# Kernel optimization log

Measured on AMD Instinct MI355X. Metric: run time of the kernel, lower is better.

The kernel has to match this reference:

```python
import jax, jax.numpy as jnp
import numpy as np

B, S, D, H = 4, 2048, 1024, 16
DK = D // H
EPS = 1e-5


def setup_inputs() -> dict:
    key = jax.random.key(0)
    ks = jax.random.split(key, 9)
    lim = 1.0 / np.sqrt(DK)  # nn.Linear default init range
    def u(k, shape):
        return jax.random.uniform(k, shape, jnp.float32, -lim, lim)
    return {
        "x": jax.random.normal(ks[0], (B, S, D), jnp.float32),
        "Wq": u(ks[1], (H, DK, DK)),
        "bq": u(ks[2], (H, DK)),
        "Wk": u(ks[3], (H, DK, DK)),
        "bk": u(ks[4], (H, DK)),
        "Wv": u(ks[5], (H, DK, DK)),
        "bv": u(ks[6], (H, DK)),
        "gamma": jnp.ones((D,), jnp.float32),
        "beta": jnp.zeros((D,), jnp.float32),
    }


def reference(x, Wq, bq, Wk, bk, Wv, bv, gamma, beta):
    b, s, d = x.shape
    h, dk = Wq.shape[0], Wq.shape[1]
    xh = x.reshape(b, s, h, dk)  # chunk along feature dim -> per-head slices
    # per-head linear projections (heads batched into one einsum)
    Q = jnp.einsum("bshd,hde->bshe", xh, Wq) + bq
    K = jnp.einsum("bshd,hde->bshe", xh, Wk) + bk
    V = jnp.einsum("bshd,hde->bshe", xh, Wv) + bv
    scale = jnp.sqrt(jnp.asarray(dk, x.dtype))
    scores = jnp.einsum("bshe,bthe->bhst", Q, K) / scale  # [B,H,S,S]
    causal = jnp.tril(jnp.ones((s, s), bool))  # apply_mask=True
    scores = jnp.where(causal, scores, -jnp.inf)
    P = jax.nn.softmax(scores, axis=-1)
    O = jnp.einsum("bhst,bthe->bshe", P, V).reshape(b, s, d)  # concat heads
    # dropout is identity in eval mode; residual + LayerNorm
    y = O + x
    mu = jnp.mean(y, axis=-1, keepdims=True)
    var = jnp.mean(jnp.square(y - mu), axis=-1, keepdims=True)
    return (y - mu) * jax.lax.rsqrt(var + EPS) * gamma + beta
```

## Files before the change

kernel.cpp:

```cpp
#include <hip/hip_runtime.h>
#include <hip/hip_bf16.h>

typedef __bf16 bf16_t;
typedef bf16_t bf16x8 __attribute__((ext_vector_type(8)));
typedef bf16_t bf16x4 __attribute__((ext_vector_type(4)));
typedef float f32x4 __attribute__((ext_vector_type(4)));

#define SEQ    2048
#define DHEAD  64
#define DMODEL 1024
#define KVB    64
#define BHN    64
#define LOG2E  1.4426950408889634f

__device__ __forceinline__ f32x4 mfma16(bf16x8 a, bf16x8 b, f32x4 c) {
  return __builtin_amdgcn_mfma_f32_16x16x32_bf16(a, b, c, 0, 0, 0);
}

__device__ __forceinline__ void gload16(void* l, const void* g) {
  __builtin_amdgcn_global_load_lds(
      (const __attribute__((address_space(1))) unsigned int*)g,
      (__attribute__((address_space(3))) unsigned int*)l,
      16, 0, 0);
}

__global__ __launch_bounds__(256) void qkv_kernel(
    const float* __restrict__ x,
    const float* __restrict__ Wq, const float* __restrict__ bq,
    const float* __restrict__ Wk, const float* __restrict__ bk,
    const float* __restrict__ Wv, const float* __restrict__ bv,
    bf16_t* __restrict__ Qw, bf16_t* __restrict__ Kw, bf16_t* __restrict__ VTw) {
  __shared__ __align__(16) char x_lds[256 * 128];
  __shared__ __align__(16) char w_lds[8192];

  const int bh = blockIdx.y;
  const int b = bh >> 4, h = bh & 15;
  const int s0 = blockIdx.x * 256;
  const int t = threadIdx.x;
  const int w = t >> 6, lane = t & 63;
  const int lo = lane & 15, g = lane >> 4;

#pragma unroll
  for (int p = 0; p < 8; ++p) {
    const int row = p * 32 + (t >> 3);
    const int c = t & 7;
    const float* xp = x + ((size_t)(b * SEQ + s0 + row)) * DMODEL + h * DHEAD + c * 8;
    const float4 f0 = *(const float4*)xp;
    const float4 f1 = *(const float4*)(xp + 4);
    bf16x8 v;
    v[0] = (bf16_t)f0.x; v[1] = (bf16_t)f0.y; v[2] = (bf16_t)f0.z; v[3] = (bf16_t)f0.w;
    v[4] = (bf16_t)f1.x; v[5] = (bf16_t)f1.y; v[6] = (bf16_t)f1.z; v[7] = (bf16_t)f1.w;
    *(bf16x8*)(x_lds + row * 128 + ((c * 16) ^ ((row & 7) << 4))) = v;
  }
  __syncthreads();

  for (int wi = 0; wi < 3; ++wi) {
    const float* Wp = (wi == 0) ? Wq : (wi == 1) ? Wk : Wv;
    const float* Bp = (wi == 0) ? bq : (wi == 1) ? bk : bv;
    bf16_t* Op      = (wi == 0) ? Qw : Kw;

    if (wi > 0) __syncthreads();
    {
      const int d = t >> 2, e0 = (t & 3) * 16;
      const float* wp = Wp + (size_t)(h * 64 + d) * 64 + e0;
      const float4 f0 = *(const float4*)(wp);
      const float4 f1 = *(const float4*)(wp + 4);
      const float4 f2 = *(const float4*)(wp + 8);
      const float4 f3 = *(const float4*)(wp + 12);
      float vals[16];
      vals[0] = f0.x; vals[1] = f0.y; vals[2] = f0.z; vals[3] = f0.w;
      vals[4] = f1.x; vals[5] = f1.y; vals[6] = f1.z; vals[7] = f1.w;
      vals[8] = f2.x; vals[9] = f2.y; vals[10] = f2.z; vals[11] = f2.w;
      vals[12] = f3.x; vals[13] = f3.y; vals[14] = f3.z; vals[15] = f3.w;
#pragma unroll
      for (int j = 0; j < 16; ++j) {
        const int e = e0 + j;
        *(bf16_t*)(w_lds + e * 128 + ((2 * d) ^ ((e & 7) << 4))) = (bf16_t)vals[j];
      }
    }
    __syncthreads();

    bf16x8 wf[2][4];
#pragma unroll
    for (int ct = 0; ct < 4; ++ct)
#pragma unroll
      for (int ks = 0; ks < 2; ++ks)
        wf[ks][ct] = *(const bf16x8*)(w_lds + (ct * 16 + lo) * 128 +
                                      ((ks * 64 + g * 16) ^ ((lo & 7) << 4)));
    float4 biasv[4];
    float biass[4];
    if (wi < 2) {
#pragma unroll
      for (int ct = 0; ct < 4; ++ct)
        biasv[ct] = *(const float4*)(Bp + h * 64 + ct * 16 + g * 4);
    } else {
#pragma unroll
      for (int ct = 0; ct < 4; ++ct) biass[ct] = Bp[h * 64 + ct * 16 + lo];
    }

    const float sc = (wi == 0) ? (0.125f * LOG2E) : 1.0f;
#pragma unroll
    for (int it = 0; it < 4; ++it) {
      const int r0 = it * 64 + w * 16;
      bf16x8 xa[2];
#pragma unroll
      for (int ks = 0; ks < 2; ++ks) {
        const int row = r0 + lo;
        xa[ks] = *(const bf16x8*)(x_lds + row * 128 +
                                  ((ks * 64 + g * 16) ^ ((row & 7) << 4)));
      }
      if (wi < 2) {
#pragma unroll
        for (int ct = 0; ct < 4; ++ct) {
          f32x4 a = (f32x4){0.f, 0.f, 0.f, 0.f};
          a = mfma16(wf[0][ct], xa[0], a);
          a = mfma16(wf[1][ct], xa[1], a);
          bf16x4 pk;
#pragma unroll
          for (int r = 0; r < 4; ++r)
            pk[r] = (bf16_t)((a[r] + ((const float*)&biasv[ct])[r]) * sc);
          *(bf16x4*)(Op + ((size_t)bh * SEQ + s0 + r0 + lo) * DHEAD + ct * 16 + g * 4) = pk;
        }
      } else {
#pragma unroll
        for (int ct = 0; ct < 4; ++ct) {
          f32x4 a = (f32x4){0.f, 0.f, 0.f, 0.f};
          a = mfma16(xa[0], wf[0][ct], a);
          a = mfma16(xa[1], wf[1][ct], a);
          bf16x4 pk;
#pragma unroll
          for (int r = 0; r < 4; ++r) pk[r] = (bf16_t)(a[r] + biass[ct]);
          *(bf16x4*)(VTw + ((size_t)bh * DHEAD + ct * 16 + lo) * SEQ + s0 + r0 + g * 4) = pk;
        }
      }
    }
  }
}

__global__ __launch_bounds__(256, 4) void attn_kernel(
    const bf16_t* __restrict__ Qw, const bf16_t* __restrict__ Kw,
    const bf16_t* __restrict__ VTw, float* __restrict__ Out) {
  __shared__ __align__(16) char stage_lds[2][16384];
  __shared__ __align__(16) char p_lds[4][2048];

  const int f = blockIdx.x;
  const int bh = (f & 7) * 8 + ((f >> 3) & 7);
  const int pair = f >> 6;
  const int b = bh >> 4, h = bh & 15;

  const int t = threadIdx.x;
  const int w = t >> 6, lane = t & 63;
  const int lo = lane & 15, g = lane >> 4;
  char* pbase = &p_lds[w][0];

  const int strow = w * 8 + (lane >> 3);
  const int scol = ((lane & 7) * 16) ^ ((lane >> 3) << 4);
  const char* Kbase = (const char*)(Kw + (size_t)bh * SEQ * DHEAD);
  const char* Vbase = (const char*)(VTw + (size_t)bh * DHEAD * SEQ);
  const bf16_t* Qb = Qw + (size_t)bh * SEQ * DHEAD;
  const int swz = (lo & 7) << 4;

  for (int half = 0; half < 2; ++half) {
    const int qt = half ? (31 - pair) : pair;
    const int q0 = qt * 64;
    const int qw0 = q0 + w * 16;
    const int kts = qt + 1;

    bf16x8 qf[2];
    {
      const bf16_t* qp = Qb + (size_t)(qw0 + lo) * DHEAD + g * 8;
      qf[0] = *(const bf16x8*)(qp);
      qf[1] = *(const bf16x8*)(qp + 32);
    }
    float m_run = -1e30f, l_run = 0.f;
    f32x4 oacc[4];
#pragma unroll
    for (int dt = 0; dt < 4; ++dt) oacc[dt] = (f32x4){0.f, 0.f, 0.f, 0.f};

    __syncthreads();
    {
      char* db = &stage_lds[0][0];
#pragma unroll
      for (int p = 0; p < 2; ++p) {
        gload16(db + p * 4096 + w * 1024,
                Kbase + (size_t)(p * 32 + strow) * 128 + scol);
        gload16(db + 8192 + p * 4096 + w * 1024,
                Vbase + (size_t)(p * 32 + strow) * 4096 + scol);
      }
    }
    int cur = 0;
    for (int kt = 0; kt < kts; ++kt) {
      const int kv0 = kt * KVB;
      __syncthreads();
      if (kt + 1 < kts) {
        const int nk = kv0 + KVB;
        char* db = &stage_lds[cur ^ 1][0];
#pragma unroll
        for (int p = 0; p < 2; ++p) {
          gload16(db + p * 4096 + w * 1024,
                  Kbase + (size_t)(nk + p * 32 + strow) * 128 + scol);
          gload16(db + 8192 + p * 4096 + w * 1024,
                  Vbase + (size_t)(p * 32 + strow) * 4096 + (size_t)nk * 2 + scol);
        }
      }
      const char* kb = &stage_lds[cur][0];
      const char* vb = kb + 8192;

      bf16x8 kf[2][4];
#pragma unroll
      for (int ks = 0; ks < 2; ++ks)
#pragma unroll
        for (int ct = 0; ct < 4; ++ct)
          kf[ks][ct] = *(const bf16x8*)(kb + (ct * 16 + lo) * 128 +
                                        ((ks * 64 + g * 16) ^ swz));
      f32x4 sa[4];
      __builtin_amdgcn_s_setprio(1);
#pragma unroll
      for (int ct = 0; ct < 4; ++ct) {
        f32x4 a = (f32x4){0.f, 0.f, 0.f, 0.f};
        a = mfma16(kf[0][ct], qf[0], a);
        a = mfma16(kf[1][ct], qf[1], a);
        sa[ct] = a;
      }
      __builtin_amdgcn_s_setprio(0);

      if (kt == qt) {
        const int q = qw0 + lo;
#pragma unroll
        for (int ct = 0; ct < 4; ++ct)
#pragma unroll
          for (int r = 0; r < 4; ++r) {
            const int kv = kv0 + ct * 16 + g * 4 + r;
            if (kv > q) sa[ct][r] = -1e30f;
          }
      }
      float mt = -1e30f;
#pragma unroll
      for (int ct = 0; ct < 4; ++ct)
        mt = fmaxf(mt, fmaxf(fmaxf(sa[ct][0], sa[ct][1]),
                             fmaxf(sa[ct][2], sa[ct][3])));
      mt = fmaxf(mt, __shfl_xor(mt, 16));
      mt = fmaxf(mt, __shfl_xor(mt, 32));
      if (__any(mt > m_run + 8.f)) {
        const float mn = fmaxf(m_run, mt);
        const float rs = exp2f(m_run - mn);
        l_run *= rs;
        m_run = mn;
#pragma unroll
        for (int r = 0; r < 4; ++r) {
          const float fr = __shfl(rs, g * 4 + r);
#pragma unroll
          for (int dt = 0; dt < 4; ++dt) oacc[dt][r] *= fr;
        }
      }
      float lt = 0.f;
#pragma unroll
      for (int ct = 0; ct < 4; ++ct) {
        bf16x4 pk;
#pragma unroll
        for (int r = 0; r < 4; ++r) {
          const float pv = exp2f(sa[ct][r] - m_run);
          lt += pv;
          pk[r] = (bf16_t)pv;
        }
        *(bf16x4*)(pbase + lo * 128 + ((ct * 32 + g * 8) ^ swz)) = pk;
      }
      lt += __shfl_xor(lt, 16);
      lt += __shfl_xor(lt, 32);
      l_run += lt;

      bf16x8 vf[2][4];
#pragma unroll
      for (int ks = 0; ks < 2; ++ks)
#pragma unroll
        for (int dt = 0; dt < 4; ++dt)
          vf[ks][dt] = *(const bf16x8*)(vb + (dt * 16 + lo) * 128 +
                                        ((ks * 64 + g * 16) ^ swz));
      __builtin_amdgcn_s_setprio(1);
#pragma unroll
      for (int ks = 0; ks < 2; ++ks) {
        const bf16x8 pa = *(const bf16x8*)(pbase + lo * 128 + ((ks * 64 + g * 16) ^ swz));
#pragma unroll
        for (int dt = 0; dt < 4; ++dt)
          oacc[dt] = mfma16(pa, vf[ks][dt], oacc[dt]);
      }
      __builtin_amdgcn_s_setprio(0);
      cur ^= 1;
    }
    const float inv = 1.f / l_run;
#pragma unroll
    for (int r = 0; r < 4; ++r) {
      const float fr = __shfl(inv, g * 4 + r);
      const int srow = qw0 + g * 4 + r;
      float* op = Out + ((size_t)b * SEQ + srow) * DMODEL + h * DHEAD;
#pragma unroll
      for (int dt = 0; dt < 4; ++dt) op[dt * 16 + lo] = oacc[dt][r] * fr;
    }
  }
}

__global__ __launch_bounds__(256) void ln_kernel(
    const float* __restrict__ x, const float* __restrict__ gamma,
    const float* __restrict__ beta, float* __restrict__ out) {
  __shared__ float red[8];
  const int row = blockIdx.x;
  const int t = threadIdx.x;
  float* orow = out + (size_t)row * DMODEL;
  const float* xrow = x + (size_t)row * DMODEL;

  const float4 o = *(const float4*)(orow + t * 4);
  const float4 xv = *(const float4*)(xrow + t * 4);
  float y0 = o.x + xv.x, y1 = o.y + xv.y, y2 = o.z + xv.z, y3 = o.w + xv.w;
  float s = y0 + y1 + y2 + y3;
  float sq = y0 * y0 + y1 * y1 + y2 * y2 + y3 * y3;
#pragma unroll
  for (int m = 1; m < 64; m <<= 1) {
    s += __shfl_xor(s, m);
    sq += __shfl_xor(sq, m);
  }
  const int w = t >> 6;
  if ((t & 63) == 0) { red[w] = s; red[4 + w] = sq; }
  __syncthreads();
  const float S = red[0] + red[1] + red[2] + red[3];
  const float SQ = red[4] + red[5] + red[6] + red[7];
  const float mu = S * (1.f / DMODEL);
  const float var = SQ * (1.f / DMODEL) - mu * mu;
  const float rstd = rsqrtf(var + 1e-5f);
  const float4 gv = *(const float4*)(gamma + t * 4);
  const float4 bv = *(const float4*)(beta + t * 4);
  float4 res;
  res.x = (y0 - mu) * rstd * gv.x + bv.x;
  res.y = (y1 - mu) * rstd * gv.y + bv.y;
  res.z = (y2 - mu) * rstd * gv.z + bv.z;
  res.w = (y3 - mu) * rstd * gv.w + bv.w;
  *(float4*)(orow + t * 4) = res;
}

extern "C" void kernel_launch(void* const* d_in, const int* in_sizes, int n_in,
                              void* d_out, int out_size, void* d_ws, size_t ws_size,
                              hipStream_t stream) {
  const float* x     = (const float*)d_in[0];
  const float* Wq    = (const float*)d_in[1];
  const float* bq    = (const float*)d_in[2];
  const float* Wk    = (const float*)d_in[3];
  const float* bk    = (const float*)d_in[4];
  const float* Wv    = (const float*)d_in[5];
  const float* bv    = (const float*)d_in[6];
  const float* gamma = (const float*)d_in[7];
  const float* beta  = (const float*)d_in[8];
  float* out = (float*)d_out;

  const size_t per = (size_t)BHN * SEQ * DHEAD;
  bf16_t* Qw  = (bf16_t*)d_ws;
  bf16_t* Kw  = Qw + per;
  bf16_t* VTw = Kw + per;

  qkv_kernel<<<dim3(8, 64), 256, 0, stream>>>(x, Wq, bq, Wk, bk, Wv, bv, Qw, Kw, VTw);
  attn_kernel<<<dim3(1024), 256, 0, stream>>>(Qw, Kw, VTw, out);
  ln_kernel<<<dim3(8192), 256, 0, stream>>>(x, gamma, beta, out);
}
```

Baseline: 198.9 us.

## Switch attention to 32x32 MFMA with 128-row query tiles and register-resident P

The attention kernel moves from 16x16x32 to 32x32x16 bf16 MFMA, with each wave owning 32 query rows. Query tiles grow to 128 rows, so the grid halves and launch bounds drop to 2 blocks per CU. P stays in registers via cvt_pk_bf16 and permlane32_swap instead of a round trip through LDS, and fully masked 32-column sub-blocks are skipped. The QKV kernel also preloads all three weight matrices into LDS up front to remove the per-weight barriers, at the cost of more LDS and registers, which lowers occupancy.

```diff
diff --git a/kernel.cpp b/kernel.cpp
--- a/kernel.cpp
+++ b/kernel.cpp
@@ -5,16 +5,29 @@
 typedef bf16_t bf16x8 __attribute__((ext_vector_type(8)));
 typedef bf16_t bf16x4 __attribute__((ext_vector_type(4)));
 typedef float f32x4 __attribute__((ext_vector_type(4)));
+typedef float f32x16 __attribute__((ext_vector_type(16)));
+typedef unsigned int u32;
+typedef u32 u32x4 __attribute__((ext_vector_type(4)));
 
 #define SEQ    2048
 #define DHEAD  64
 #define DMODEL 1024
-#define KVB    64
 #define BHN    64
 #define LOG2E  1.4426950408889634f
+#define NEGBIG (-1e30f)
+#define MASKV  (-1e38f)
 
 __device__ __forceinline__ f32x4 mfma16(bf16x8 a, bf16x8 b, f32x4 c) {
   return __builtin_amdgcn_mfma_f32_16x16x32_bf16(a, b, c, 0, 0, 0);
+}
+__device__ __forceinline__ f32x16 mfma32(bf16x8 a, bf16x8 b, f32x16 c) {
+  return __builtin_amdgcn_mfma_f32_32x32x16_bf16(a, b, c, 0, 0, 0);
+}
+__device__ __forceinline__ f32x16 zero16() {
+  f32x16 z;
+#pragma unroll
+  for (int i = 0; i < 16; ++i) z[i] = 0.f;
+  return z;
 }
 
 __device__ __forceinline__ void gload16(void* l, const void* g) {
@@ -31,7 +44,7 @@
     const float* __restrict__ Wv, const float* __restrict__ bv,
     bf16_t* __restrict__ Qw, bf16_t* __restrict__ Kw, bf16_t* __restrict__ VTw) {
   __shared__ __align__(16) char x_lds[256 * 128];
-  __shared__ __align__(16) char w_lds[8192];
+  __shared__ __align__(16) char w_lds[3][8192];
 
   const int bh = blockIdx.y;
   const int b = bh >> 4, h = bh & 15;
@@ -40,6 +53,26 @@
   const int w = t >> 6, lane = t & 63;
   const int lo = lane & 15, g = lane >> 4;
 
+#pragma unroll
+  for (int wi = 0; wi < 3; ++wi) {
+    const float* Wp = (wi == 0) ? Wq : (wi == 1) ? Wk : Wv;
+    const int d = t >> 2, e0 = (t & 3) * 16;
+    const float* wp = Wp + (size_t)(h * 64 + d) * 64 + e0;
+    const float4 f0 = *(const float4*)(wp);
+    const float4 f1 = *(const float4*)(wp + 4);
+    const float4 f2 = *(const float4*)(wp + 8);
+    const float4 f3 = *(const float4*)(wp + 12);
+    float vals[16];
+    vals[0] = f0.x; vals[1] = f0.y; vals[2] = f0.z; vals[3] = f0.w;
+    vals[4] = f1.x; vals[5] = f1.y; vals[6] = f1.z; vals[7] = f1.w;
+    vals[8] = f2.x; vals[9] = f2.y; vals[10] = f2.z; vals[11] = f2.w;
+    vals[12] = f3.x; vals[13] = f3.y; vals[14] = f3.z; vals[15] = f3.w;
+#pragma unroll
+    for (int j = 0; j < 16; ++j) {
+      const int e = e0 + j;
+      *(bf16_t*)(w_lds[wi] + e * 128 + ((2 * d) ^ ((e & 7) << 4))) = (bf16_t)vals[j];
+    }
+  }
 #pragma unroll
   for (int p = 0; p < 8; ++p) {
     const int row = p * 32 + (t >> 3);
@@ -54,38 +87,17 @@
   }
   __syncthreads();
 
+#pragma unroll
   for (int wi = 0; wi < 3; ++wi) {
-    const float* Wp = (wi == 0) ? Wq : (wi == 1) ? Wk : Wv;
     const float* Bp = (wi == 0) ? bq : (wi == 1) ? bk : bv;
     bf16_t* Op      = (wi == 0) ? Qw : Kw;
 
-    if (wi > 0) __syncthreads();
-    {
-      const int d = t >> 2, e0 = (t & 3) * 16;
-      const float* wp = Wp + (size_t)(h * 64 + d) * 64 + e0;
-      const float4 f0 = *(const float4*)(wp);
-      const float4 f1 = *(const float4*)(wp + 4);
-      const float4 f2 = *(const float4*)(wp + 8);
-      const float4 f3 = *(const float4*)(wp + 12);
-      float vals[16];
-      vals[0] = f0.x; vals[1] = f0.y; vals[2] = f0.z; vals[3] = f0.w;
-      vals[4] = f1.x; vals[5] = f1.y; vals[6] = f1.z; vals[7] = f1.w;
-      vals[8] = f2.x; vals[9] = f2.y; vals[10] = f2.z; vals[11] = f2.w;
-      vals[12] = f3.x; vals[13] = f3.y; vals[14] = f3.z; vals[15] = f3.w;
-#pragma unroll
-      for (int j = 0; j < 16; ++j) {
-        const int e = e0 + j;
-        *(bf16_t*)(w_lds + e * 128 + ((2 * d) ^ ((e & 7) << 4))) = (bf16_t)vals[j];
-      }
-    }
-    __syncthreads();
-
     bf16x8 wf[2][4];
 #pragma unroll
     for (int ct = 0; ct < 4; ++ct)
 #pragma unroll
       for (int ks = 0; ks < 2; ++ks)
-        wf[ks][ct] = *(const bf16x8*)(w_lds + (ct * 16 + lo) * 128 +
+        wf[ks][ct] = *(const bf16x8*)(w_lds[wi] + (ct * 16 + lo) * 128 +
                                       ((ks * 64 + g * 16) ^ ((lo & 7) << 4)));
     float4 biasv[4];
     float biass[4];
@@ -137,11 +149,10 @@
   }
 }
 
-__global__ __launch_bounds__(256, 4) void attn_kernel(
+__global__ __launch_bounds__(256, 2) void attn_kernel(
     const bf16_t* __restrict__ Qw, const bf16_t* __restrict__ Kw,
     const bf16_t* __restrict__ VTw, float* __restrict__ Out) {
   __shared__ __align__(16) char stage_lds[2][16384];
-  __shared__ __align__(16) char p_lds[4][2048];
 
   const int f = blockIdx.x;
   const int bh = (f & 7) * 8 + ((f >> 3) & 7);
@@ -150,152 +161,177 @@
 
   const int t = threadIdx.x;
   const int w = t >> 6, lane = t & 63;
-  const int lo = lane & 15, g = lane >> 4;
-  char* pbase = &p_lds[w][0];
-
-  const int strow = w * 8 + (lane >> 3);
-  const int scol = ((lane & 7) * 16) ^ ((lane >> 3) << 4);
+  const int l31 = lane & 31, hi = lane >> 5;
+
   const char* Kbase = (const char*)(Kw + (size_t)bh * SEQ * DHEAD);
   const char* Vbase = (const char*)(VTw + (size_t)bh * DHEAD * SEQ);
   const bf16_t* Qb = Qw + (size_t)bh * SEQ * DHEAD;
-  const int swz = (lo & 7) << 4;
 
   for (int half = 0; half < 2; ++half) {
-    const int qt = half ? (31 - pair) : pair;
-    const int q0 = qt * 64;
-    const int qw0 = q0 + w * 16;
-    const int kts = qt + 1;
-
-    bf16x8 qf[2];
-    {
-      const bf16_t* qp = Qb + (size_t)(qw0 + lo) * DHEAD + g * 8;
-      qf[0] = *(const bf16x8*)(qp);
-      qf[1] = *(const bf16x8*)(qp + 32);
-    }
-    float m_run = -1e30f, l_run = 0.f;
-    f32x4 oacc[4];
-#pragma unroll
-    for (int dt = 0; dt < 4; ++dt) oacc[dt] = (f32x4){0.f, 0.f, 0.f, 0.f};
+    const int qt = half ? (15 - pair) : pair;
+    const int qw0 = qt * 128 + w * 32;
+    const int qabs = qw0 + l31;
+    const int kts = 2 * qt + 2;
+
+    bf16x8 qf[4];
+#pragma unroll
+    for (int kk = 0; kk < 4; ++kk)
+      qf[kk] = *(const bf16x8*)(Qb + (size_t)qabs * DHEAD + kk * 16 + hi * 8);
+
+    float m = NEGBIG, l = 0.f;
+    f32x16 oacc[2];
+    oacc[0] = zero16();
+    oacc[1] = zero16();
 
     __syncthreads();
     {
       char* db = &stage_lds[0][0];
 #pragma unroll
       for (int p = 0; p < 2; ++p) {
-        gload16(db + p * 4096 + w * 1024,
-                Kbase + (size_t)(p * 32 + strow) * 128 + scol);
-        gload16(db + 8192 + p * 4096 + w * 1024,
-                Vbase + (size_t)(p * 32 + strow) * 4096 + scol);
+        const int c = w * 2 + p;
+        gload16(db + c * 1024, Kbase + (size_t)lane * 128 + c * 16);
+        gload16(db + 8192 + c * 1024, Vbase + (size_t)lane * 4096 + c * 16);
       }
     }
     int cur = 0;
     for (int kt = 0; kt < kts; ++kt) {
-      const int kv0 = kt * KVB;
+      const int kv0 = kt * 64;
       __syncthreads();
       if (kt + 1 < kts) {
-        const int nk = kv0 + KVB;
         char* db = &stage_lds[cur ^ 1][0];
+        const int nk = kv0 + 64;
 #pragma unroll
         for (int p = 0; p < 2; ++p) {
-          gload16(db + p * 4096 + w * 1024,
-                  Kbase + (size_t)(nk + p * 32 + strow) * 128 + scol);
-          gload16(db + 8192 + p * 4096 + w * 1024,
-                  Vbase + (size_t)(p * 32 + strow) * 4096 + (size_t)nk * 2 + scol);
-        }
-      }
+          const int c = w * 2 + p;
+          gload16(db + c * 1024, Kbase + (size_t)(nk + lane) * 128 + c * 16);
+          gload16(db + 8192 + c * 1024,
+                  Vbase + (size_t)lane * 4096 + (size_t)nk * 2 + c * 16);
+        }
+      }
+      const bool live0 = (kv0 <= qw0 + 31);
+      const bool live1 = (kv0 + 32 <= qw0 + 31);
+      if (!live0) { cur ^= 1; continue; }
       const char* kb = &stage_lds[cur][0];
       const char* vb = kb + 8192;
 
-      bf16x8 kf[2][4];
-#pragma unroll
-      for (int ks = 0; ks < 2; ++ks)
-#pragma unroll
-        for (int ct = 0; ct < 4; ++ct)
-          kf[ks][ct] = *(const bf16x8*)(kb + (ct * 16 + lo) * 128 +
-                                        ((ks * 64 + g * 16) ^ swz));
-      f32x4 sa[4];
+      f32x16 sa0 = zero16(), sa1 = zero16();
       __builtin_amdgcn_s_setprio(1);
 #pragma unroll
-      for (int ct = 0; ct < 4; ++ct) {
-        f32x4 a = (f32x4){0.f, 0.f, 0.f, 0.f};
-        a = mfma16(kf[0][ct], qf[0], a);
-        a = mfma16(kf[1][ct], qf[1], a);
-        sa[ct] = a;
+      for (int kk = 0; kk < 4; ++kk) {
+        const bf16x8 kf = *(const bf16x8*)(kb + (kk * 2 + hi) * 1024 + l31 * 16);
+        sa0 = mfma32(kf, qf[kk], sa0);
+      }
+      if (live1) {
+#pragma unroll
+        for (int kk = 0; kk < 4; ++kk) {
+          const bf16x8 kf = *(const bf16x8*)(kb + (kk * 2 + hi) * 1024 + (32 + l31) * 16);
+          sa1 = mfma32(kf, qf[kk], sa1);
+        }
       }
       __builtin_amdgcn_s_setprio(0);
 
-      if (kt == qt) {
-        const int q = qw0 + lo;
-#pragma unroll
-        for (int ct = 0; ct < 4; ++ct)
-#pragma unroll
-          for (int r = 0; r < 4; ++r) {
-            const int kv = kv0 + ct * 16 + g * 4 + r;
-            if (kv > q) sa[ct][r] = -1e30f;
-          }
-      }
-      float mt = -1e30f;
-#pragma unroll
-      for (int ct = 0; ct < 4; ++ct)
-        mt = fmaxf(mt, fmaxf(fmaxf(sa[ct][0], sa[ct][1]),
-                             fmaxf(sa[ct][2], sa[ct][3])));
-      mt = fmaxf(mt, __shfl_xor(mt, 16));
+      if (kv0 + 31 > qw0) {
+#pragma unroll
+        for (int j = 0; j < 16; ++j) {
+          const int kvj = kv0 + 4 * hi + ((j & 3) + 8 * (j >> 2));
+          if (kvj > qabs) sa0[j] = MASKV;
+        }
+      }
+      if (live1 && kv0 + 63 > qw0) {
+#pragma unroll
+        for (int j = 0; j < 16; ++j) {
+          const int kvj = kv0 + 32 + 4 * hi + ((j & 3) + 8 * (j >> 2));
+          if (kvj > qabs) sa1[j] = MASKV;
+        }
+      }
+
+      float mt = NEGBIG;
+#pragma unroll
+      for (int j = 0; j < 16; ++j) mt = fmaxf(mt, sa0[j]);
+      if (live1) {
+#pragma unroll
+        for (int j = 0; j < 16; ++j) mt = fmaxf(mt, sa1[j]);
+      }
       mt = fmaxf(mt, __shfl_xor(mt, 32));
-      if (__any(mt > m_run + 8.f)) {
-        const float mn = fmaxf(m_run, mt);
-        const float rs = exp2f(m_run - mn);
-        l_run *= rs;
-        m_run = mn;
-#pragma unroll
-        for (int r = 0; r < 4; ++r) {
-          const float fr = __shfl(rs, g * 4 + r);
-#pragma unroll
-          for (int dt = 0; dt < 4; ++dt) oacc[dt][r] *= fr;
-        }
-      }
+      if (__any(mt > m + 8.f)) {
+        const float mn = fmaxf(m, mt);
+        const float rs = exp2f(m - mn);
+        l *= rs;
+        m = mn;
+#pragma unroll
+        for (int i = 0; i < 16; ++i) { oacc[0][i] *= rs; oacc[1][i] *= rs; }
+      }
+
+      u32 wds0[8], wds1[8];
       float lt = 0.f;
 #pragma unroll
-      for (int ct = 0; ct < 4; ++ct) {
-        bf16x4 pk;
-#pragma unroll
-        for (int r = 0; r < 4; ++r) {
-          const float pv = exp2f(sa[ct][r] - m_run);
-          lt += pv;
-          pk[r] = (bf16_t)pv;
-        }
-        *(bf16x4*)(pbase + lo * 128 + ((ct * 32 + g * 8) ^ swz)) = pk;
-      }
-      lt += __shfl_xor(lt, 16);
-      lt += __shfl_xor(lt, 32);
-      l_run += lt;
-
-      bf16x8 vf[2][4];
-#pragma unroll
-      for (int ks = 0; ks < 2; ++ks)
-#pragma unroll
-        for (int dt = 0; dt < 4; ++dt)
-          vf[ks][dt] = *(const bf16x8*)(vb + (dt * 16 + lo) * 128 +
-                                        ((ks * 64 + g * 16) ^ swz));
+      for (int a2 = 0; a2 < 8; ++a2) {
+        const float p0 = exp2f(sa0[2 * a2] - m);
+        const float p1 = exp2f(sa0[2 * a2 + 1] - m);
+        lt += p0 + p1;
+        asm("v_cvt_pk_bf16_f32 %0, %1, %2" : "=v"(wds0[a2]) : "v"(p0), "v"(p1));
+      }
+      if (live1) {
+#pragma unroll
+        for (int a2 = 0; a2 < 8; ++a2) {
+          const float p0 = exp2f(sa1[2 * a2] - m);
+          const float p1 = exp2f(sa1[2 * a2 + 1] - m);
+          lt += p0 + p1;
+          asm("v_cvt_pk_bf16_f32 %0, %1, %2" : "=v"(wds1[a2]) : "v"(p0), "v"(p1));
+        }
+      }
+      l += lt;
+
+      bf16x8 pb[4];
+      {
+        asm("v_permlane32_swap_b32 %0, %1" : "+v"(wds0[0]), "+v"(wds0[2]));
+        asm("v_permlane32_swap_b32 %0, %1" : "+v"(wds0[1]), "+v"(wds0[3]));
+        asm("v_permlane32_swap_b32 %0, %1" : "+v"(wds0[4]), "+v"(wds0[6]));
+        asm("v_permlane32_swap_b32 %0, %1" : "+v"(wds0[5]), "+v"(wds0[7]));
+        u32x4 b0 = {wds0[0], wds0[1], wds0[2], wds0[3]};
+        u32x4 b1 = {wds0[4], wds0[5], wds0[6], wds0[7]};
+        pb[0] = __builtin_bit_cast(bf16x8, b0);
+        pb[1] = __builtin_bit_cast(bf16x8, b1);
+      }
+      if (live1) {
+        asm("v_permlane32_swap_b32 %0, %1" : "+v"(wds1[0]), "+v"(wds1[2]));
+        asm("v_permlane32_swap_b32 %0, %1" : "+v"(wds1[1]), "+v"(wds1[3]));
+        asm("v_permlane32_swap_b32 %0, %1" : "+v"(wds1[4]), "+v"(wds1[6]));
+        asm("v_permlane32_swap_b32 %0, %1" : "+v"(wds1[5]), "+v"(wds1[7]));
+        u32x4 b2 = {wds1[0], wds1[1], wds1[2], wds1[3]};
+        u32x4 b3 = {wds1[4], wds1[5], wds1[6], wds1[7]};
+        pb[2] = __builtin_bit_cast(bf16x8, b2);
+        pb[3] = __builtin_bit_cast(bf16x8, b3);
+      }
+
       __builtin_amdgcn_s_setprio(1);
 #pragma unroll
-      for (int ks = 0; ks < 2; ++ks) {
-        const bf16x8 pa = *(const bf16x8*)(pbase + lo * 128 + ((ks * 64 + g * 16) ^ swz));
-#pragma unroll
-        for (int dt = 0; dt < 4; ++dt)
-          oacc[dt] = mfma16(pa, vf[ks][dt], oacc[dt]);
+      for (int kk = 0; kk < 4; ++kk) {
+        if (kk >= 2 && !live1) continue;
+#pragma unroll
+        for (int dt = 0; dt < 2; ++dt) {
+          const bf16x8 vf =
+              *(const bf16x8*)(vb + (kk * 2 + hi) * 1024 + (dt * 32 + l31) * 16);
+          oacc[dt] = mfma32(vf, pb[kk], oacc[dt]);
+        }
       }
       __builtin_amdgcn_s_setprio(0);
       cur ^= 1;
     }
-    const float inv = 1.f / l_run;
-#pragma unroll
-    for (int r = 0; r < 4; ++r) {
-      const float fr = __shfl(inv, g * 4 + r);
-      const int srow = qw0 + g * 4 + r;
-      float* op = Out + ((size_t)b * SEQ + srow) * DMODEL + h * DHEAD;
-#pragma unroll
-      for (int dt = 0; dt < 4; ++dt) op[dt * 16 + lo] = oacc[dt][r] * fr;
-    }
+
+    const float linv = 1.0f / (l + __shfl_xor(l, 32));
+    float* orow = Out + ((size_t)b * SEQ + qabs) * DMODEL + h * DHEAD;
+#pragma unroll
+    for (int dt = 0; dt < 2; ++dt)
+#pragma unroll
+      for (int rr = 0; rr < 4; ++rr) {
+        float4 v;
+        v.x = oacc[dt][rr * 4 + 0] * linv;
+        v.y = oacc[dt][rr * 4 + 1] * linv;
+        v.z = oacc[dt][rr * 4 + 2] * linv;
+        v.w = oacc[dt][rr * 4 + 3] * linv;
+        *(float4*)(orow + dt * 32 + rr * 8 + hi * 4) = v;
+      }
   }
 }
 
@@ -314,9 +350,9 @@
   float s = y0 + y1 + y2 + y3;
   float sq = y0 * y0 + y1 * y1 + y2 * y2 + y3 * y3;
 #pragma unroll
-  for (int m = 1; m < 64; m <<= 1) {
-    s += __shfl_xor(s, m);
-    sq += __shfl_xor(sq, m);
+  for (int mm = 1; mm < 64; mm <<= 1) {
+    s += __shfl_xor(s, mm);
+    sq += __shfl_xor(sq, mm);
   }
   const int w = t >> 6;
   if ((t & 63) == 0) { red[w] = s; red[4 + w] = sq; }
@@ -356,6 +392,6 @@
   bf16_t* VTw = Kw + per;
 
   qkv_kernel<<<dim3(8, 64), 256, 0, stream>>>(x, Wq, bq, Wk, bk, Wv, bv, Qw, Kw, VTw);
-  attn_kernel<<<dim3(1024), 256, 0, stream>>>(Qw, Kw, VTw, out);
+  attn_kernel<<<dim3(512), 256, 0, stream>>>(Qw, Kw, VTw, out);
   ln_kernel<<<dim3(8192), 256, 0, stream>>>(x, gamma, beta, out);
 }
```

Result: faster. 192.3 us (-3.3%).
